# Performance work log

Hardware: AMD Instinct MI355X
Metric: run time of the kernel (lower is better)

The kernel has to match this reference:

```python
import jax, jax.numpy as jnp
import numpy as np

ALPHA = 0.2          # LeakyReLU negative slope
NEG_INF = -9e15      # mask value used by the original module


def setup_inputs() -> dict:
    key = jax.random.key(0)
    k1, k2, k3, k4 = jax.random.split(key, 4)
    N, Din, Dout = 8192, 512, 256
    features = jax.random.normal(k1, (N, Din), dtype=jnp.float32)
    adj = jax.random.randint(k2, (N, N), 0, 2, dtype=jnp.int32)
    W = jax.random.normal(k3, (Din, Dout), dtype=jnp.float32) * (1.414 / np.sqrt(Din))
    a = jax.random.normal(k4, (2 * Dout, 1), dtype=jnp.float32) * (1.414 / np.sqrt(2 * Dout))
    return {"features": features, "adj": adj, "W": W, "a": a}


def reference(features, adj, W, a):
    Dout = W.shape[1]
    Wh = features @ W                       # [N, Dout]
    # e_ij = leakyrelu([Wh_i || Wh_j] @ a) decomposes additively:
    # identical math to the N*N*2D concat in the original, without materializing it.
    src = Wh @ a[:Dout, 0]                  # [N]  contribution of node i
    dst = Wh @ a[Dout:, 0]                  # [N]  contribution of node j
    e = jax.nn.leaky_relu(src[:, None] + dst[None, :], negative_slope=ALPHA)  # [N, N]
    masked = jnp.where(adj > 0, e, NEG_INF)
    attention = jax.nn.softmax(masked, axis=1)   # dropout p=0.0 (eval) -> identity
    h_prime = attention @ Wh                # [N, Dout]
    return jax.nn.elu(h_prime)
```

## Files before the change

kernel.cpp:

```cpp
#include <hip/hip_runtime.h>
#include <hip/hip_bf16.h>

#define NN   8192
#define DIN  512
#define DOUT 256

typedef __attribute__((ext_vector_type(8)))  short s16x8;
typedef __attribute__((ext_vector_type(16))) float f32x16;

static __device__ __forceinline__ unsigned short f2bf(float f) {
    union { float f; unsigned u; } v; v.f = f;
    unsigned r = v.u + 0x7fffu + ((v.u >> 16) & 1u);
    return (unsigned short)(r >> 16);
}

static __device__ __forceinline__ void gload_lds16(const void* g, void* l) {
    __builtin_amdgcn_global_load_lds(
        (const __attribute__((address_space(1))) unsigned int*)g,
        (__attribute__((address_space(3))) unsigned int*)l, 16, 0, 0);
}

__global__ __launch_bounds__(256) void k_wh2(const float* __restrict__ feat,
                                             const float* __restrict__ W,
                                             const float* __restrict__ a,
                                             unsigned short* __restrict__ WhT,
                                             float* __restrict__ src,
                                             float* __restrict__ dst) {
    __shared__ float lf[16 * DIN];
    __shared__ float red[2][4][16];
    const int tid = threadIdx.x;
    const int i0  = blockIdx.x * 16;
    const int w   = tid >> 6, lane = tid & 63;

    const float4* fsrc = (const float4*)(feat + (size_t)i0 * DIN);
    float4* fdst = (float4*)lf;
    #pragma unroll
    for (int q = 0; q < 8; ++q) fdst[tid + q * 256] = fsrc[tid + q * 256];
    __syncthreads();

    const int c = tid;
    float outs[16];
    #pragma unroll
    for (int r = 0; r < 16; ++r) outs[r] = 0.f;

    for (int k = 0; k < DIN; k += 4) {
        float w0 = W[(k + 0) * DOUT + c];
        float w1 = W[(k + 1) * DOUT + c];
        float w2 = W[(k + 2) * DOUT + c];
        float w3 = W[(k + 3) * DOUT + c];
        #pragma unroll
        for (int r = 0; r < 16; ++r) {
            float4 f = *(const float4*)&lf[r * DIN + k];
            outs[r] = fmaf(f.x, w0, fmaf(f.y, w1, fmaf(f.z, w2, fmaf(f.w, w3, outs[r]))));
        }
    }

    unsigned short tb[16];
    #pragma unroll
    for (int r = 0; r < 16; ++r) tb[r] = f2bf(outs[r]);
    uint4* wt = (uint4*)(WhT + (size_t)c * NN + i0);
    wt[0] = *(uint4*)&tb[0];
    wt[1] = *(uint4*)&tb[8];

    const float as_ = a[c], ad_ = a[DOUT + c];
    #pragma unroll
    for (int r = 0; r < 16; ++r) {
        float s = outs[r] * as_;
        float d = outs[r] * ad_;
        #pragma unroll
        for (int off = 32; off; off >>= 1) {
            s += __shfl_xor(s, off);
            d += __shfl_xor(d, off);
        }
        if (lane == 0) { red[0][w][r] = s; red[1][w][r] = d; }
    }
    __syncthreads();
    if (tid < 16)
        src[i0 + tid] = red[0][0][tid] + red[0][1][tid] + red[0][2][tid] + red[0][3][tid];
    else if (tid < 32) {
        int r = tid - 16;
        dst[i0 + r] = red[1][0][r] + red[1][1][r] + red[1][2][r] + red[1][3][r];
    }
}

__global__ __launch_bounds__(256) void k_mask(const int* __restrict__ adj,
                                              unsigned char* __restrict__ bits) {
    const int row = blockIdx.x;
    const int tid = threadIdx.x;
    const int* base = adj + (size_t)row * NN + tid * 32;
    unsigned int u = 0;
    #pragma unroll
    for (int j = 0; j < 8; ++j) {
        int4 v = *(const int4*)(base + j * 4);
        unsigned int b = (v.x > 0 ? 1u : 0u) | (v.y > 0 ? 2u : 0u) |
                         (v.z > 0 ? 4u : 0u) | (v.w > 0 ? 8u : 0u);
        u |= b << (j * 4);
    }
    *(unsigned int*)(bits + (size_t)row * 1024 + tid * 4) = u;
}

#define STEP9(T, PA, PB)                                                                 \
{                                                                                        \
                    \
    {                                                                                    \
        const size_t koff_ = (size_t)(((T) + 1 <= 15) ? (T) + 1 : 15) * 128;             \
        _Pragma("unroll")                                                                \
        for (int q = 0; q < 8; ++q)                                                      \
            gload_lds16(gB + (size_t)q * (32 * NN * 2) + koff_,                          \
                        Bs[((T) + 1) & 1] + q * 4096 + tid * 16);                        \
    }                                                                                    \
                                              \
    unsigned long long m64_ = 0;                                                         \
    float4 dv_[8];                                                                       \
    if ((T) < 15) {                                                                      \
        m64_ = brow64[(T) + 1];                                                          \
        _Pragma("unroll")                                                                \
        for (int ks4 = 0; ks4 < 4; ++ks4) {                                              \
            dv_[2 * ks4]     = *(const float4*)(dstk + ((T) + 1) * 64 + ks4 * 16 + lhi8);\
            dv_[2 * ks4 + 1] = *(const float4*)(dstk + ((T) + 1) * 64 + ks4 * 16 + lhi8 + 4);\
        }                                                                                \
    }                                                                                    \
                                                  \
    __builtin_amdgcn_s_setprio(1);                                                       \
    _Pragma("unroll")                                                                    \
    for (int ks4 = 0; ks4 < 4; ++ks4) {                                                  \
        _Pragma("unroll")                                                                \
        for (int ct = 0; ct < 8; ++ct) {                                                 \
            const int brow_ = ct * 32 + l31;                                             \
            s16x8 bfv_ = *(const s16x8*)(Bs[(T) & 1] + brow_ * 128 +                     \
                                         ((ks4 * 32 + lhi * 16) ^ ((brow_ & 7) << 4)));  \
            acc[ct] = __builtin_amdgcn_mfma_f32_32x32x16_bf16(PA[ks4], bfv_, acc[ct], 0, 0, 0); \
        }                                                                                \
    }                                                                                    \
    __builtin_amdgcn_s_setprio(0);                                                       \
                                 \
    if ((T) < 15) {                                                                      \
        const float* df_ = (const float*)dv_;                                            \
        _Pragma("unroll")                                                                \
        for (int ks4 = 0; ks4 < 4; ++ks4) {                                              \
            const unsigned int m8_ = (unsigned int)(m64_ >> (ks4 * 16 + lhi8)) & 0xffu;  \
            s16x8 pw_;                                                                   \
            _Pragma("unroll")                                                            \
            for (int jj = 0; jj < 8; ++jj) {                                             \
                float x_ = si + df_[ks4 * 8 + jj];                                       \
                x_ = fmaxf(x_, 0.2f * x_);                           \
                float p_ = (m8_ >> jj) & 1u ? __expf(x_) : 0.f;      \
                den += p_;                                                               \
                pw_[jj] = (short)f2bf(p_);                                               \
            }                                                                            \
            PB[ks4] = pw_;                                                               \
        }                                                                                \
    }                                                                                    \
    asm volatile("s_waitcnt vmcnt(0) lgkmcnt(0)" ::: "memory");                          \
    __builtin_amdgcn_s_barrier();                                                        \
    __builtin_amdgcn_sched_barrier(0);                                                   \
}

__global__ __launch_bounds__(256, 2) void k_attn9(const unsigned char* __restrict__ bits,
                                                  const unsigned short* __restrict__ WhT,
                                                  const float* __restrict__ src,
                                                  const float* __restrict__ dstg,
                                                  float* __restrict__ denp,
                                                  float* __restrict__ part) {
    __shared__ __attribute__((aligned(16))) char Bs[2][32768];

    const int tid  = threadIdx.x;
    const int lane = tid & 63;
    const int wv   = tid >> 6;
    const int l31  = lane & 31, lhi = lane >> 5;
    const int lhi8 = lhi * 8;

    const int ks  = blockIdx.x & 7;
    const int rt  = blockIdx.x >> 3;
    const int kb0 = ks * 1024;

    const int gr  = rt * 128 + wv * 32 + l31;
    const float si = src[gr];
    const unsigned long long* brow64 =
        (const unsigned long long*)(bits + (size_t)gr * 1024 + ks * 128);
    const float* dstk = dstg + kb0;

    const int c0 = tid >> 3;
    const char* gB = (const char*)WhT + ((size_t)c0 * NN + kb0) * 2
                   + (((tid & 7) * 16) ^ ((c0 & 7) << 4));

    f32x16 acc[8];
    #pragma unroll
    for (int ct = 0; ct < 8; ++ct)
        #pragma unroll
        for (int e = 0; e < 16; ++e) acc[ct][e] = 0.f;
    float den = 0.f;

    s16x8 pA[4], pB[4];

    #pragma unroll
    for (int q = 0; q < 8; ++q)
        gload_lds16(gB + (size_t)q * (32 * NN * 2), Bs[0] + q * 4096 + tid * 16);
    {
        const unsigned long long m64 = brow64[0];
        #pragma unroll
        for (int ks4 = 0; ks4 < 4; ++ks4) {
            float4 d0 = *(const float4*)(dstk + ks4 * 16 + lhi8);
            float4 d1 = *(const float4*)(dstk + ks4 * 16 + lhi8 + 4);
            const float df[8] = {d0.x, d0.y, d0.z, d0.w, d1.x, d1.y, d1.z, d1.w};
            const unsigned int m8 = (unsigned int)(m64 >> (ks4 * 16 + lhi8)) & 0xffu;
            s16x8 pw;
            #pragma unroll
            for (int jj = 0; jj < 8; ++jj) {
                float x = si + df[jj];
                x = fmaxf(x, 0.2f * x);
                float p = (m8 >> jj) & 1u ? __expf(x) : 0.f;
                den += p;
                pw[jj] = (short)f2bf(p);
            }
            pA[ks4] = pw;
        }
    }
    asm volatile("s_waitcnt vmcnt(0) lgkmcnt(0)" ::: "memory");
    __builtin_amdgcn_s_barrier();
    __builtin_amdgcn_sched_barrier(0);

    #pragma unroll
    for (int tt = 0; tt < 8; ++tt) {
        STEP9(2 * tt,     pA, pB);
        STEP9(2 * tt + 1, pB, pA);
    }

    den += __shfl_xor(den, 32);
    if (lhi == 0) denp[(size_t)ks * NN + gr] = den;

    float* pp = part + (size_t)ks * (NN * DOUT);
    #pragma unroll
    for (int ct = 0; ct < 8; ++ct) {
        #pragma unroll
        for (int e = 0; e < 16; ++e) {
            const int row = rt * 128 + wv * 32 + (e & 3) + 8 * (e >> 2) + 4 * lhi;
            pp[(size_t)row * DOUT + ct * 32 + l31] = acc[ct][e];
        }
    }
}

__global__ __launch_bounds__(256) void k_finish3(const float* __restrict__ part,
                                                 const float* __restrict__ denp,
                                                 float* __restrict__ out) {
    const int idx = blockIdx.x * 256 + threadIdx.x;
    const int row = idx >> 6;
    float den = 0.f;
    #pragma unroll
    for (int i = 0; i < 8; ++i) den += denp[(size_t)i * NN + row];
    float rv = den > 0.f ? 1.f / den : 0.f;
    const size_t st = (size_t)NN * DOUT / 4;
    const float4* p = (const float4*)part;
    float sx = 0.f, sy = 0.f, sz = 0.f, sw = 0.f;
    #pragma unroll
    for (int i = 0; i < 8; ++i) {
        float4 v = p[idx + i * st];
        sx += v.x; sy += v.y; sz += v.z; sw += v.w;
    }
    float4 s;
    s.x = sx * rv; s.y = sy * rv; s.z = sz * rv; s.w = sw * rv;
    s.x = s.x > 0.f ? s.x : expm1f(s.x);
    s.y = s.y > 0.f ? s.y : expm1f(s.y);
    s.z = s.z > 0.f ? s.z : expm1f(s.z);
    s.w = s.w > 0.f ? s.w : expm1f(s.w);
    ((float4*)out)[idx] = s;
}

extern "C" void kernel_launch(void* const* d_in, const int* in_sizes, int n_in,
                              void* d_out, int out_size, void* d_ws, size_t ws_size,
                              hipStream_t stream) {
    const float* feat = (const float*)d_in[0];
    const int*   adj  = (const int*)d_in[1];
    const float* W    = (const float*)d_in[2];
    const float* a    = (const float*)d_in[3];
    float* out = (float*)d_out;

    char* ws = (char*)d_ws;
    unsigned short* WhT  = (unsigned short*)ws;
    float*          src  = (float*)(ws + 4194304);
    float*          dst  = (float*)(ws + 4227072);
    float*          denp = (float*)(ws + 4259840);
    unsigned char*  bits = (unsigned char*)(ws + 4521984);
    float*          part = (float*)(ws + 12910592);

    k_mask   <<<8192, 256, 0, stream>>>(adj, bits);
    k_wh2    <<<512,  256, 0, stream>>>(feat, W, a, WhT, src, dst);
    k_attn9  <<<512,  256, 0, stream>>>(bits, WhT, src, dst, denp, part);
    k_finish3<<<2048, 256, 0, stream>>>(part, denp, out);
}
```

Baseline: 211.4 us.

## Pre-pack Wh into MFMA fragment layout and load B operands directly from global

The Wh projection kernel now writes bf16 Wh in a layout packed per 32-column tile and per 16-row k-group, matching the MFMA B-fragment lane order. The attention kernel drops the LDS double-buffer, the async global-to-LDS loads and the barriers, and has each lane read its B fragments straight from global memory in a simple per-k-step loop. The aim is to cut LDS traffic and synchronisation overhead, but the software pipelining that hid global latency is lost. The attention kernel is also launched twice, which repeats its work.

```diff
diff --git a/kernel.cpp b/kernel.cpp
--- a/kernel.cpp
+++ b/kernel.cpp
@@ -14,16 +14,10 @@
     return (unsigned short)(r >> 16);
 }
 
-static __device__ __forceinline__ void gload_lds16(const void* g, void* l) {
-    __builtin_amdgcn_global_load_lds(
-        (const __attribute__((address_space(1))) unsigned int*)g,
-        (__attribute__((address_space(3))) unsigned int*)l, 16, 0, 0);
-}
-
-__global__ __launch_bounds__(256) void k_wh2(const float* __restrict__ feat,
+__global__ __launch_bounds__(256) void k_wh3(const float* __restrict__ feat,
                                              const float* __restrict__ W,
                                              const float* __restrict__ a,
-                                             unsigned short* __restrict__ WhT,
+                                             uint4* __restrict__ Bpk,
                                              float* __restrict__ src,
                                              float* __restrict__ dst) {
     __shared__ float lf[16 * DIN];
@@ -58,9 +52,9 @@
     unsigned short tb[16];
     #pragma unroll
     for (int r = 0; r < 16; ++r) tb[r] = f2bf(outs[r]);
-    uint4* wt = (uint4*)(WhT + (size_t)c * NN + i0);
-    wt[0] = *(uint4*)&tb[0];
-    wt[1] = *(uint4*)&tb[8];
+    const int ct = c >> 5, l31c = c & 31;
+    Bpk[((size_t)ct * 512 + blockIdx.x) * 64 +  0 + l31c] = *(uint4*)&tb[0];
+    Bpk[((size_t)ct * 512 + blockIdx.x) * 64 + 32 + l31c] = *(uint4*)&tb[8];
 
     const float as_ = a[c], ad_ = a[DOUT + c];
     #pragma unroll
@@ -99,71 +93,12 @@
     *(unsigned int*)(bits + (size_t)row * 1024 + tid * 4) = u;
 }
 
-#define STEP9(T, PA, PB)                                                                 \
-{                                                                                        \
-                    \
-    {                                                                                    \
-        const size_t koff_ = (size_t)(((T) + 1 <= 15) ? (T) + 1 : 15) * 128;             \
-        _Pragma("unroll")                                                                \
-        for (int q = 0; q < 8; ++q)                                                      \
-            gload_lds16(gB + (size_t)q * (32 * NN * 2) + koff_,                          \
-                        Bs[((T) + 1) & 1] + q * 4096 + tid * 16);                        \
-    }                                                                                    \
-                                              \
-    unsigned long long m64_ = 0;                                                         \
-    float4 dv_[8];                                                                       \
-    if ((T) < 15) {                                                                      \
-        m64_ = brow64[(T) + 1];                                                          \
-        _Pragma("unroll")                                                                \
-        for (int ks4 = 0; ks4 < 4; ++ks4) {                                              \
-            dv_[2 * ks4]     = *(const float4*)(dstk + ((T) + 1) * 64 + ks4 * 16 + lhi8);\
-            dv_[2 * ks4 + 1] = *(const float4*)(dstk + ((T) + 1) * 64 + ks4 * 16 + lhi8 + 4);\
-        }                                                                                \
-    }                                                                                    \
-                                                  \
-    __builtin_amdgcn_s_setprio(1);                                                       \
-    _Pragma("unroll")                                                                    \
-    for (int ks4 = 0; ks4 < 4; ++ks4) {                                                  \
-        _Pragma("unroll")                                                                \
-        for (int ct = 0; ct < 8; ++ct) {                                                 \
-            const int brow_ = ct * 32 + l31;                                             \
-            s16x8 bfv_ = *(const s16x8*)(Bs[(T) & 1] + brow_ * 128 +                     \
-                                         ((ks4 * 32 + lhi * 16) ^ ((brow_ & 7) << 4)));  \
-            acc[ct] = __builtin_amdgcn_mfma_f32_32x32x16_bf16(PA[ks4], bfv_, acc[ct], 0, 0, 0); \
-        }                                                                                \
-    }                                                                                    \
-    __builtin_amdgcn_s_setprio(0);                                                       \
-                                 \
-    if ((T) < 15) {                                                                      \
-        const float* df_ = (const float*)dv_;                                            \
-        _Pragma("unroll")                                                                \
-        for (int ks4 = 0; ks4 < 4; ++ks4) {                                              \
-            const unsigned int m8_ = (unsigned int)(m64_ >> (ks4 * 16 + lhi8)) & 0xffu;  \
-            s16x8 pw_;                                                                   \
-            _Pragma("unroll")                                                            \
-            for (int jj = 0; jj < 8; ++jj) {                                             \
-                float x_ = si + df_[ks4 * 8 + jj];                                       \
-                x_ = fmaxf(x_, 0.2f * x_);                           \
-                float p_ = (m8_ >> jj) & 1u ? __expf(x_) : 0.f;      \
-                den += p_;                                                               \
-                pw_[jj] = (short)f2bf(p_);                                               \
-            }                                                                            \
-            PB[ks4] = pw_;                                                               \
-        }                                                                                \
-    }                                                                                    \
-    asm volatile("s_waitcnt vmcnt(0) lgkmcnt(0)" ::: "memory");                          \
-    __builtin_amdgcn_s_barrier();                                                        \
-    __builtin_amdgcn_sched_barrier(0);                                                   \
-}
-
-__global__ __launch_bounds__(256, 2) void k_attn9(const unsigned char* __restrict__ bits,
-                                                  const unsigned short* __restrict__ WhT,
-                                                  const float* __restrict__ src,
-                                                  const float* __restrict__ dstg,
-                                                  float* __restrict__ denp,
-                                                  float* __restrict__ part) {
-    __shared__ __attribute__((aligned(16))) char Bs[2][32768];
-
+__global__ __launch_bounds__(256, 2) void k_attn10(const unsigned char* __restrict__ bits,
+                                                   const uint4* __restrict__ Bpk,
+                                                   const float* __restrict__ src,
+                                                   const float* __restrict__ dstg,
+                                                   float* __restrict__ denp,
+                                                   float* __restrict__ part) {
     const int tid  = threadIdx.x;
     const int lane = tid & 63;
     const int wv   = tid >> 6;
@@ -172,17 +107,12 @@
 
     const int ks  = blockIdx.x & 7;
     const int rt  = blockIdx.x >> 3;
-    const int kb0 = ks * 1024;
+    const int ktg0 = ks * 64;
 
     const int gr  = rt * 128 + wv * 32 + l31;
     const float si = src[gr];
-    const unsigned long long* brow64 =
-        (const unsigned long long*)(bits + (size_t)gr * 1024 + ks * 128);
-    const float* dstk = dstg + kb0;
-
-    const int c0 = tid >> 3;
-    const char* gB = (const char*)WhT + ((size_t)c0 * NN + kb0) * 2
-                   + (((tid & 7) * 16) ^ ((c0 & 7) << 4));
+    const unsigned char* bb = bits + (size_t)gr * 1024 + ks * 128;
+    const float* dk = dstg + ks * 1024 + lhi8;
 
     f32x16 acc[8];
     #pragma unroll
@@ -191,39 +121,32 @@
         for (int e = 0; e < 16; ++e) acc[ct][e] = 0.f;
     float den = 0.f;
 
-    s16x8 pA[4], pB[4];
-
-    #pragma unroll
-    for (int q = 0; q < 8; ++q)
-        gload_lds16(gB + (size_t)q * (32 * NN * 2), Bs[0] + q * 4096 + tid * 16);
-    {
-        const unsigned long long m64 = brow64[0];
-        #pragma unroll
-        for (int ks4 = 0; ks4 < 4; ++ks4) {
-            float4 d0 = *(const float4*)(dstk + ks4 * 16 + lhi8);
-            float4 d1 = *(const float4*)(dstk + ks4 * 16 + lhi8 + 4);
-            const float df[8] = {d0.x, d0.y, d0.z, d0.w, d1.x, d1.y, d1.z, d1.w};
-            const unsigned int m8 = (unsigned int)(m64 >> (ks4 * 16 + lhi8)) & 0xffu;
-            s16x8 pw;
-            #pragma unroll
-            for (int jj = 0; jj < 8; ++jj) {
-                float x = si + df[jj];
-                x = fmaxf(x, 0.2f * x);
-                float p = (m8 >> jj) & 1u ? __expf(x) : 0.f;
-                den += p;
-                pw[jj] = (short)f2bf(p);
-            }
-            pA[ks4] = pw;
-        }
-    }
-    asm volatile("s_waitcnt vmcnt(0) lgkmcnt(0)" ::: "memory");
-    __builtin_amdgcn_s_barrier();
-    __builtin_amdgcn_sched_barrier(0);
-
-    #pragma unroll
-    for (int tt = 0; tt < 8; ++tt) {
-        STEP9(2 * tt,     pA, pB);
-        STEP9(2 * tt + 1, pB, pA);
+    for (int t = 0; t < 64; ++t) {
+        s16x8 bf[8];
+        #pragma unroll
+        for (int ct = 0; ct < 8; ++ct) {
+            uint4 v = Bpk[((size_t)ct * 512 + ktg0 + t) * 64 + lane];
+            bf[ct] = *(s16x8*)&v;
+        }
+        const unsigned int m16 = *(const unsigned short*)(bb + t * 2);
+        const unsigned int m8  = (m16 >> lhi8) & 0xffu;
+        float4 d0 = *(const float4*)(dk + t * 16);
+        float4 d1 = *(const float4*)(dk + t * 16 + 4);
+        const float df[8] = {d0.x, d0.y, d0.z, d0.w, d1.x, d1.y, d1.z, d1.w};
+        s16x8 pa;
+        #pragma unroll
+        for (int jj = 0; jj < 8; ++jj) {
+            float x = si + df[jj];
+            x = fmaxf(x, 0.2f * x);
+            float p = (m8 >> jj) & 1u ? __expf(x) : 0.f;
+            den += p;
+            pa[jj] = (short)f2bf(p);
+        }
+        __builtin_amdgcn_s_setprio(1);
+        #pragma unroll
+        for (int ct = 0; ct < 8; ++ct)
+            acc[ct] = __builtin_amdgcn_mfma_f32_32x32x16_bf16(pa, bf[ct], acc[ct], 0, 0, 0);
+        __builtin_amdgcn_s_setprio(0);
     }
 
     den += __shfl_xor(den, 32);
@@ -276,15 +199,16 @@
     float* out = (float*)d_out;
 
     char* ws = (char*)d_ws;
-    unsigned short* WhT  = (unsigned short*)ws;
+    uint4*          Bpk  = (uint4*)ws;
     float*          src  = (float*)(ws + 4194304);
     float*          dst  = (float*)(ws + 4227072);
     float*          denp = (float*)(ws + 4259840);
     unsigned char*  bits = (unsigned char*)(ws + 4521984);
     float*          part = (float*)(ws + 12910592);
 
-    k_mask   <<<8192, 256, 0, stream>>>(adj, bits);
-    k_wh2    <<<512,  256, 0, stream>>>(feat, W, a, WhT, src, dst);
-    k_attn9  <<<512,  256, 0, stream>>>(bits, WhT, src, dst, denp, part);
+    k_mask  <<<8192, 256, 0, stream>>>(adj, bits);
+    k_wh3   <<<512,  256, 0, stream>>>(feat, W, a, Bpk, src, dst);
+    k_attn10<<<512,  256, 0, stream>>>(bits, Bpk, src, dst, denp, part);
+    k_attn10<<<512,  256, 0, stream>>>(bits, Bpk, src, dst, denp, part);
     k_finish3<<<2048, 256, 0, stream>>>(part, denp, out);
 }
```

Measured after the change: 301.4 us. 42.6% more time.
